# Optimization experiments

Measured on AMD Instinct MI355X. Metric: run time of the kernel, lower is better.

## Reference

```python
import jax, jax.numpy as jnp
import numpy as np

B, S, D, H = 4, 2048, 1024, 16
HD = D // H
FF = 4 * D
EPS = 1e-5


def setup_inputs() -> dict:
    key = jax.random.key(0)
    ks = jax.random.split(key, 12)
    s = lambda fan_in: 1.0 / np.sqrt(fan_in)
    inp = {
        "x": jax.random.normal(ks[0], (B, S, D), dtype=jnp.float32),
        # attention weights stored as (d_in, d_out)
        "Wq": jax.random.normal(ks[1], (D, D), dtype=jnp.float32) * s(D),
        "Wk": jax.random.normal(ks[2], (D, D), dtype=jnp.float32) * s(D),
        "Wv": jax.random.normal(ks[3], (D, D), dtype=jnp.float32) * s(D),
        "Wo": jax.random.normal(ks[4], (D, D), dtype=jnp.float32) * s(D),
        "bo": jnp.zeros((D,), dtype=jnp.float32),
        # feed-forward
        "W1": jax.random.normal(ks[5], (D, FF), dtype=jnp.float32) * s(D),
        "b1": jnp.zeros((FF,), dtype=jnp.float32),
        "W2": jax.random.normal(ks[6], (FF, D), dtype=jnp.float32) * s(FF),
        "b2": jnp.zeros((D,), dtype=jnp.float32),
        # layernorms
        "g1": jnp.ones((D,), dtype=jnp.float32),
        "be1": jnp.zeros((D,), dtype=jnp.float32),
        "g2": jnp.ones((D,), dtype=jnp.float32),
        "be2": jnp.zeros((D,), dtype=jnp.float32),
    }
    return inp


def _layernorm(x, gamma, beta):
    mean = jnp.mean(x, axis=-1, keepdims=True)
    var = jnp.mean(jnp.square(x - mean), axis=-1, keepdims=True)  # unbiased=False
    return gamma * (x - mean) / jnp.sqrt(var + EPS) + beta


def _gelu_tanh(x):
    c = jnp.sqrt(jnp.asarray(2.0 / jnp.pi, dtype=x.dtype))
    return 0.5 * x * (1.0 + jnp.tanh(c * (x + 0.044715 * x * x * x)))


def _block(x, Wq, Wk, Wv, Wo, bo, W1, b1, W2, b2, g1, be1, g2, be2):
    # --- pre-LN causal multi-head attention ---
    shortcut = x
    h = _layernorm(x, g1, be1)
    q = (h @ Wq).reshape(B, S, H, HD).transpose(0, 2, 1, 3)  # [B,H,S,HD]
    k = (h @ Wk).reshape(B, S, H, HD).transpose(0, 2, 1, 3)
    v = (h @ Wv).reshape(B, S, H, HD).transpose(0, 2, 1, 3)
    scores = jnp.einsum("bhqd,bhkd->bhqk", q, k)
    causal = jnp.tril(jnp.ones((S, S), dtype=bool))  # True = keep
    scores = jnp.where(causal, scores, -jnp.inf)
    attn = jax.nn.softmax(scores / jnp.sqrt(jnp.asarray(HD, scores.dtype)), axis=-1)
    ctx = jnp.einsum("bhqk,bhkd->bqhd", attn, v).reshape(B, S, D)
    x = ctx @ Wo + bo + shortcut
    # --- pre-LN GELU MLP ---
    shortcut = x
    h = _layernorm(x, g2, be2)
    h = _gelu_tanh(h @ W1 + b1) @ W2 + b2
    return h + shortcut


def reference(x, Wq, Wk, Wv, Wo, bo, W1, b1, W2, b2, g1, be1, g2, be2):
    return _block(x, Wq, Wk, Wv, Wo, bo, W1, b1, W2, b2, g1, be1, g2, be2)
```

## Files before the change

### kernel.cpp

```cpp
#include <hip/hip_runtime.h>
#include <cstdint>

#define B_   4
#define S_   2048
#define D_   1024
#define H_   16
#define HD_  64
#define FF_  4096
#define MTOK 8192

typedef short s16x8 __attribute__((ext_vector_type(8), may_alias));
typedef float f32x4 __attribute__((ext_vector_type(4)));
typedef unsigned short u16x4 __attribute__((ext_vector_type(4), may_alias));
typedef unsigned short u16x8 __attribute__((ext_vector_type(8), may_alias));

#define GLD_LDS16(g, l)                                                  \
  __builtin_amdgcn_global_load_lds(                                      \
      (__attribute__((address_space(1))) void*)(g),                      \
      (__attribute__((address_space(3))) void*)(l), 16, 0, 0)

__device__ __forceinline__ unsigned short f2bf(float f) {
  unsigned u = __float_as_uint(f);
  unsigned r = 0x7fffu + ((u >> 16) & 1u);
  return (unsigned short)((u + r) >> 16);
}

__global__ __launch_bounds__(256) void k_transpose(const float* __restrict__ in,
                                                   unsigned short* __restrict__ out,
                                                   int R, int C) {
  __shared__ float tile[32][33];
  int tx = threadIdx.x, ty = threadIdx.y;
  int c0 = blockIdx.x * 32, r0 = blockIdx.y * 32;
#pragma unroll
  for (int j = 0; j < 4; ++j)
    tile[ty + j * 8][tx] = in[(size_t)(r0 + ty + j * 8) * C + (c0 + tx)];
  __syncthreads();
#pragma unroll
  for (int j = 0; j < 4; ++j)
    out[(size_t)(c0 + ty + j * 8) * R + (r0 + tx)] = f2bf(tile[tx][ty + j * 8]);
}

__global__ __launch_bounds__(256) void k_layernorm(const float* __restrict__ x,
                                                   const float* __restrict__ g,
                                                   const float* __restrict__ be,
                                                   unsigned short* __restrict__ out) {
  int row = blockIdx.x, t = threadIdx.x;
  const float4* xr = (const float4*)(x + (size_t)row * D_);
  float4 v = xr[t];
  float s = v.x + v.y + v.z + v.w;
  float q = v.x * v.x + v.y * v.y + v.z * v.z + v.w * v.w;
#pragma unroll
  for (int o = 1; o < 64; o <<= 1) { s += __shfl_xor(s, o); q += __shfl_xor(q, o); }
  __shared__ float red[8];
  int wid = t >> 6;
  if ((t & 63) == 0) { red[wid * 2] = s; red[wid * 2 + 1] = q; }
  __syncthreads();
  s = red[0] + red[2] + red[4] + red[6];
  q = red[1] + red[3] + red[5] + red[7];
  float mean = s * (1.0f / D_);
  float rstd = rsqrtf(q * (1.0f / D_) - mean * mean + 1e-5f);
  float4 gv = ((const float4*)g)[t];
  float4 bv = ((const float4*)be)[t];
  u16x4 o4;
  o4[0] = f2bf(gv.x * (v.x - mean) * rstd + bv.x);
  o4[1] = f2bf(gv.y * (v.y - mean) * rstd + bv.y);
  o4[2] = f2bf(gv.z * (v.z - mean) * rstd + bv.z);
  o4[3] = f2bf(gv.w * (v.w - mean) * rstd + bv.w);
  *(u16x4*)(out + (size_t)row * D_ + t * 4) = o4;
}

template <int MODE>
__global__ __launch_bounds__(512, 2) void k_gemm8p(
    const unsigned short* __restrict__ A, const unsigned short* __restrict__ Bt,
    const float* __restrict__ bias,
    unsigned short* __restrict__ outb,
    int M, int N, int K) {
  __shared__ __align__(16) unsigned short smem[8 * 8192];
  unsigned short* const Rs = smem;

  const int tid = threadIdx.x;
  const int wid = tid >> 6, lane = tid & 63;
  const int l16 = lane & 15, lg = lane >> 4;
  const int wr = wid >> 2, wc = wid & 3;
  const int nwg = gridDim.x * gridDim.y;
  const int id = blockIdx.y * gridDim.x + blockIdx.x;
  const int swz = (id & 7) * (nwg >> 3) + (id >> 3);
  const int m0 = (swz / gridDim.x) * 256, n0 = (swz % gridDim.x) * 256;

  f32x4 acc[8][4];
#pragma unroll
  for (int m = 0; m < 8; ++m)
#pragma unroll
    for (int n = 0; n < 4; ++n) acc[m][n] = (f32x4)0.0f;

  const int sRow = tid >> 3;
  const int sC = (((tid & 7) ^ (sRow & 7)) << 3);
  const unsigned short* aS0 = A + (size_t)(m0 + sRow) * K + sC;
  const unsigned short* aS1 = A + (size_t)(m0 + 64 + sRow) * K + sC;
  const unsigned short* aS2 = A + (size_t)(m0 + 128 + sRow) * K + sC;
  const unsigned short* aS3 = A + (size_t)(m0 + 192 + sRow) * K + sC;
  const unsigned short* bS0 = Bt + (size_t)(n0 + sRow) * K + sC;
  const unsigned short* bS1 = Bt + (size_t)(n0 + 64 + sRow) * K + sC;
  const unsigned short* bS2 = Bt + (size_t)(n0 + 128 + sRow) * K + sC;
  const unsigned short* bS3 = Bt + (size_t)(n0 + 192 + sRow) * K + sC;
  const int d0 = tid * 16, d1 = tid * 16 + 8192;

  const int cS0 = ((lg ^ (l16 & 7)) << 3);
  const int cS1 = (((4 + lg) ^ (l16 & 7)) << 3);

  const int nt = K / 64;

  GLD_LDS16(aS0, (char*)(smem + 0 * 8192) + d0);
  GLD_LDS16(aS1, (char*)(smem + 0 * 8192) + d1);
  GLD_LDS16(bS0, (char*)(smem + 1 * 8192) + d0);
  GLD_LDS16(bS1, (char*)(smem + 1 * 8192) + d1);
  GLD_LDS16(bS2, (char*)(smem + 2 * 8192) + d0);
  GLD_LDS16(bS3, (char*)(smem + 2 * 8192) + d1);
  GLD_LDS16(aS2, (char*)(smem + 3 * 8192) + d0);
  GLD_LDS16(aS3, (char*)(smem + 3 * 8192) + d1);
  asm volatile("s_waitcnt vmcnt(4)" ::: "memory");
  __builtin_amdgcn_sched_barrier(0);
  __builtin_amdgcn_s_barrier();

#define PHASE(P, WSTR, DOSTAGE)                                                \
  {                                                                            \
    constexpr int mq_ = (P) >> 1, nh_ = (P) & 1;                               \
    const unsigned short* Au = smem + ((kt & 1) * 4 + (mq_ ? 3 : 0)) * 8192;   \
    const unsigned short* Bu = smem + ((kt & 1) * 4 + 1 + nh_) * 8192;         \
    s16x8 af[4][2], bf[2][2];                                                  \
    _Pragma("unroll")                                                          \
    for (int m4 = 0; m4 < 4; ++m4) {                                           \
      const unsigned short* pr_ = Au + (wr * 64 + m4 * 16 + l16) * 64;         \
      af[m4][0] = *(const s16x8*)(pr_ + cS0);                                  \
      af[m4][1] = *(const s16x8*)(pr_ + cS1);                                  \
    }                                                                          \
    _Pragma("unroll")                                                          \
    for (int n2 = 0; n2 < 2; ++n2) {                                           \
      const unsigned short* pr_ = Bu + (wc * 32 + n2 * 16 + l16) * 64;         \
      bf[n2][0] = *(const s16x8*)(pr_ + cS0);                                  \
      bf[n2][1] = *(const s16x8*)(pr_ + cS1);                                  \
    }                                                                          \
    if (DOSTAGE) {                                                             \
      char* dst_ = (char*)(smem + (((kt + 1) & 1) * 4 + (P)) * 8192);          \
      const size_t ko_ = (size_t)(kt + 1) * 64;                                \
      if constexpr ((P) == 0) {                                                \
        GLD_LDS16(aS0 + ko_, dst_ + d0); GLD_LDS16(aS1 + ko_, dst_ + d1);      \
      } else if constexpr ((P) == 1) {                                         \
        GLD_LDS16(bS0 + ko_, dst_ + d0); GLD_LDS16(bS1 + ko_, dst_ + d1);      \
      } else if constexpr ((P) == 2) {                                         \
        GLD_LDS16(bS2 + ko_, dst_ + d0); GLD_LDS16(bS3 + ko_, dst_ + d1);      \
      } else {                                                                 \
        GLD_LDS16(aS2 + ko_, dst_ + d0); GLD_LDS16(aS3 + ko_, dst_ + d1);      \
      }                                                                        \
    }                                                                          \
    asm volatile("s_waitcnt lgkmcnt(0)" ::: "memory");                         \
    __builtin_amdgcn_sched_barrier(0);                                         \
    __builtin_amdgcn_s_setprio(1);                                             \
    _Pragma("unroll")                                                          \
    for (int m4 = 0; m4 < 4; ++m4)                                             \
      _Pragma("unroll")                                                        \
      for (int n2 = 0; n2 < 2; ++n2) {                                         \
        acc[mq_ * 4 + m4][nh_ * 2 + n2] = __builtin_amdgcn_mfma_f32_16x16x32_bf16( \
            af[m4][0], bf[n2][0], acc[mq_ * 4 + m4][nh_ * 2 + n2], 0, 0, 0);   \
        acc[mq_ * 4 + m4][nh_ * 2 + n2] = __builtin_amdgcn_mfma_f32_16x16x32_bf16( \
            af[m4][1], bf[n2][1], acc[mq_ * 4 + m4][nh_ * 2 + n2], 0, 0, 0);   \
      }                                                                        \
    __builtin_amdgcn_s_setprio(0);                                             \
    asm volatile("s_waitcnt vmcnt(" WSTR ")" ::: "memory");                    \
    __builtin_amdgcn_sched_barrier(0);                                         \
    __builtin_amdgcn_s_barrier();                                              \
  }

  for (int kt = 0; kt < nt - 1; ++kt) {
    PHASE(0, "4", true)
    PHASE(1, "4", true)
    PHASE(2, "4", true)
    PHASE(3, "4", true)
  }
  {
    const int kt = nt - 1;
    PHASE(0, "2", false)
    PHASE(1, "0", false)
    PHASE(2, "0", false)
    PHASE(3, "0", false)
  }
#undef PHASE

#define RM_FLUSH8(DSTPTR, NSTRIDE, COLBASE, XFORM)                             \
  {                                                                            \
    _Pragma("unroll")                                                          \
    for (int pr = 0; pr < 4; ++pr) {                                           \
      if (wr == (pr & 1)) {                                                    \
        const int mb_ = (pr >> 1) * 4;                                         \
        _Pragma("unroll")                                                      \
        for (int nn = 0; nn < 4; ++nn) {                                       \
          const int col = (nn >> 1) * 128 + wc * 32 + (nn & 1) * 16 + l16;     \
          _Pragma("unroll")                                                    \
          for (int m4 = 0; m4 < 4; ++m4) {                                     \
            _Pragma("unroll")                                                  \
            for (int r = 0; r < 4; ++r) {                                      \
              float xv = acc[mb_ + m4][nn][r];                                 \
              XFORM;                                                           \
              Rs[(m4 * 16 + lg * 4 + r) * 264 + col] = f2bf(xv);               \
            }                                                                  \
          }                                                                    \
        }                                                                      \
      }                                                                        \
      __syncthreads();                                                         \
      const int row_l = tid >> 3;                                              \
      _Pragma("unroll")                                                        \
      for (int j = 0; j < 4; ++j) {                                            \
        const int c = (tid & 7) * 4 + j;                                       \
        u16x8 vv = *(const u16x8*)(Rs + row_l * 264 + c * 8);                  \
        *(u16x8*)((DSTPTR) + (size_t)(m0 + pr * 64 + row_l) * (NSTRIDE) +      \
                  (COLBASE) + c * 8) = vv;                                     \
      }                                                                        \
      if (pr < 3) __syncthreads();                                             \
    }                                                                          \
  }

  if constexpr (MODE == 1) {
    RM_FLUSH8(outb, N, n0, {
      xv += bias[n0 + col];
      float uu = 0.7978845608028654f * (xv + 0.044715f * xv * xv * xv);
      xv = xv * __builtin_amdgcn_rcpf(1.0f + __builtin_amdgcn_exp2f(uu * -2.885390081777927f));
    });
    return;
  }

  if constexpr (MODE == 3) {
    unsigned short* qout = outb;
    unsigned short* kout = outb + (size_t)MTOK * D_;
    unsigned short* vout = outb + 2 * (size_t)MTOK * D_;
    if (n0 < 1024) {
      RM_FLUSH8(qout, D_, n0, { xv *= 0.125f; });
    } else if (n0 < 2048) {
      RM_FLUSH8(kout, D_, n0 - 1024, {});
    } else {
      const int vbase = (m0 >> 11) * 1024 + (n0 - 2048);
      const int srow0 = m0 & 2047;
#pragma unroll
      for (int cg = 0; cg < 4; ++cg) {
        if ((wc >> 1) == (cg & 1)) {
          const int nhh = (cg >> 1) * 2;
#pragma unroll
          for (int n2 = 0; n2 < 2; ++n2) {
            const int colL = (wc & 1) * 32 + n2 * 16 + l16;
#pragma unroll
            for (int m = 0; m < 8; ++m) {
              const int rowL = (m >> 2) * 128 + wr * 64 + (m & 3) * 16 + lg * 4;
              u16x4 pk;
#pragma unroll
              for (int r = 0; r < 4; ++r) pk[r] = f2bf(acc[m][nhh + n2][r]);
              *(u16x4*)(Rs + colL * 264 + rowL) = pk;
            }
          }
        }
        __syncthreads();
        const int colf = tid >> 3;
#pragma unroll
        for (int j = 0; j < 4; ++j) {
          u16x8 vv = *(const u16x8*)(Rs + colf * 264 + (tid & 7) * 32 + j * 8);
          *(u16x8*)(vout + (size_t)(vbase + cg * 64 + colf) * S_ + srow0 +
                    (tid & 7) * 32 + j * 8) = vv;
        }
        if (cg < 3) __syncthreads();
      }
    }
    return;
  }
#undef RM_FLUSH8
}

template <int MODE>
__global__ __launch_bounds__(512, 2) void k_gemmdp(
    const unsigned short* __restrict__ A, const unsigned short* __restrict__ Bt,
    const float* __restrict__ bias, const float* __restrict__ resid,
    unsigned short* __restrict__ outb, float* __restrict__ outf,
    int M, int N, int K) {
  constexpr int BM = 128, BN = 256, BK = 64;
  constexpr int AE = BM * BK;
  constexpr int BE = BN * BK;
  constexpr int BUF_E = AE + BE;
  __shared__ __align__(16) unsigned short smem[3 * BUF_E];

  const int tid = threadIdx.x;
  const int wid = tid >> 6, lane = tid & 63;
  const int l16 = lane & 15, lg = lane >> 4;
  const int wr = wid >> 2, wc = wid & 3;
  const int nwg = gridDim.x * gridDim.y;
  const int id = blockIdx.y * gridDim.x + blockIdx.x;
  const int swz = (id & 7) * (nwg >> 3) + (id >> 3);
  const int m0 = (swz / gridDim.x) * BM, n0 = (swz % gridDim.x) * BN;

  f32x4 acc[4][4];
#pragma unroll
  for (int m = 0; m < 4; ++m)
#pragma unroll
    for (int n = 0; n < 4; ++n) acc[m][n] = (f32x4)0.0f;

  const unsigned short* aSrc[2]; int aDstB[2];
  const unsigned short* bSrc[4]; int bDstB[4];
#pragma unroll
  for (int g = 0; g < 2; ++g) {
    int q = g * 512 + tid, row = q >> 3, c = q & 7;
    aSrc[g] = A + (size_t)(m0 + row) * K + ((c ^ (row & 7)) << 3);
    aDstB[g] = q * 16;
  }
#pragma unroll
  for (int g = 0; g < 4; ++g) {
    int q = g * 512 + tid, row = q >> 3, c = q & 7;
    bSrc[g] = Bt + (size_t)(n0 + row) * K + ((c ^ (row & 7)) << 3);
    bDstB[g] = q * 16;
  }
  int cSw[2];
  cSw[0] = ((lg) ^ (l16 & 7)) * 8;
  cSw[1] = ((4 + lg) ^ (l16 & 7)) * 8;
  const int aRow = (wr * 64 + l16) * BK;
  const int bRow = (wc * 64 + l16) * BK;

#define STAGE(ti)                                                              \
  {                                                                            \
    const int _b = (ti) % 3;                                                   \
    char* _pa = (char*)(smem + _b * BUF_E);                                    \
    char* _pb = (char*)(smem + _b * BUF_E + AE);                               \
    const int _kt = (ti) * BK;                                                 \
    _Pragma("unroll")                                                          \
    for (int g = 0; g < 2; ++g) GLD_LDS16(aSrc[g] + _kt, _pa + aDstB[g]);      \
    _Pragma("unroll")                                                          \
    for (int g = 0; g < 4; ++g) GLD_LDS16(bSrc[g] + _kt, _pb + bDstB[g]);      \
  }

  const int nt = K / BK;
  STAGE(0); STAGE(1);
  asm volatile("s_waitcnt vmcnt(6)" ::: "memory");
  __builtin_amdgcn_sched_barrier(0);
  __builtin_amdgcn_s_barrier();

  for (int i = 0; i < nt; ++i) {
    if (i + 2 < nt) STAGE(i + 2);
    const unsigned short* pa = smem + (i % 3) * BUF_E + aRow;
    const unsigned short* pb = smem + (i % 3) * BUF_E + AE + bRow;
    s16x8 af[4][2], bfr[4][2];
#pragma unroll
    for (int m = 0; m < 4; ++m) {
      af[m][0] = *(const s16x8*)(pa + m * 16 * BK + cSw[0]);
      af[m][1] = *(const s16x8*)(pa + m * 16 * BK + cSw[1]);
    }
#pragma unroll
    for (int n = 0; n < 4; ++n) {
      bfr[n][0] = *(const s16x8*)(pb + n * 16 * BK + cSw[0]);
      bfr[n][1] = *(const s16x8*)(pb + n * 16 * BK + cSw[1]);
    }
    asm volatile("s_waitcnt lgkmcnt(0)" ::: "memory");
    __builtin_amdgcn_sched_barrier(0);
    __builtin_amdgcn_s_setprio(1);
#pragma unroll
    for (int m = 0; m < 4; ++m)
#pragma unroll
      for (int n = 0; n < 4; ++n) {
        acc[m][n] = __builtin_amdgcn_mfma_f32_16x16x32_bf16(af[m][0], bfr[n][0], acc[m][n], 0, 0, 0);
        acc[m][n] = __builtin_amdgcn_mfma_f32_16x16x32_bf16(af[m][1], bfr[n][1], acc[m][n], 0, 0, 0);
      }
    __builtin_amdgcn_s_setprio(0);
    if (i < nt - 2) {
      asm volatile("s_waitcnt vmcnt(6)" ::: "memory");
    } else if (i == nt - 2) {
      asm volatile("s_waitcnt vmcnt(0)" ::: "memory");
    }
    __builtin_amdgcn_sched_barrier(0);
    __builtin_amdgcn_s_barrier();
  }
#undef STAGE

  if constexpr (MODE == 2) {
#pragma unroll
    for (int n = 0; n < 4; ++n) {
      const int col = n0 + wc * 64 + n * 16 + l16;
      const float bv = bias[col];
#pragma unroll
      for (int m = 0; m < 4; ++m)
#pragma unroll
        for (int r = 0; r < 4; ++r) {
          const int row = m0 + wr * 64 + m * 16 + lg * 4 + r;
          outf[(size_t)row * N + col] = acc[m][n][r] + bv + resid[(size_t)row * N + col];
        }
    }
  }
  (void)outb;
}

__global__ __launch_bounds__(256, 3) void k_attn(
    const unsigned short* __restrict__ qg, const unsigned short* __restrict__ kg,
    const unsigned short* __restrict__ vtg, unsigned short* __restrict__ ctx) {
  const int id = blockIdx.x;
  const int bh = (id & 7) + 8 * (id >> 7);
  const int p  = (id >> 3) & 15;
  const int qtA = p, qtB = 31 - p;
  const int tid = threadIdx.x, wid = tid >> 6, lane = tid & 63;
  const int l16 = lane & 15, lg = lane >> 4;
  __shared__ __align__(16) unsigned short Ks[2][64 * 64];
  __shared__ __align__(16) unsigned short Vs[2][64 * 64];
  __shared__ __align__(16) unsigned short Ps[4][2][16 * 72];

  const size_t headoff = (size_t)(bh >> 4) * ((size_t)S_ * D_) + (size_t)(bh & 15) * HD_;
  const unsigned short* Kb = kg + headoff;
  const unsigned short* Vt = vtg + (size_t)bh * ((size_t)HD_ * S_);

  const int qrowA = qtA * 64 + wid * 16 + l16;
  const int qrowB = qtB * 64 + wid * 16 + l16;
  s16x8 qfA0 = *(const s16x8*)(qg + headoff + (size_t)qrowA * D_ + lg * 8);
  s16x8 qfA1 = *(const s16x8*)(qg + headoff + (size_t)qrowA * D_ + 32 + lg * 8);
  s16x8 qfB0 = *(const s16x8*)(qg + headoff + (size_t)qrowB * D_ + lg * 8);
  s16x8 qfB1 = *(const s16x8*)(qg + headoff + (size_t)qrowB * D_ + 32 + lg * 8);

  f32x4 oA[4], oB[4];
#pragma unroll
  for (int n = 0; n < 4; ++n) { oA[n] = (f32x4)0.0f; oB[n] = (f32x4)0.0f; }
  float lsumA[4] = {0.f, 0.f, 0.f, 0.f};
  float lsumB[4] = {0.f, 0.f, 0.f, 0.f};
  unsigned short* psA = &Ps[wid][0][0];
  unsigned short* psB = &Ps[wid][1][0];
  const int myrowA = qtA * 64 + wid * 16 + lg * 4;
  const int myrowB = qtB * 64 + wid * 16 + lg * 4;
  const float L2E = 1.4426950408889634f;

  const unsigned short* kSrc[2];
  const unsigned short* vSrc[2];
  int dstOff[2];
#pragma unroll
  for (int i = 0; i < 2; ++i) {
    int chunk = (i * 4 + wid) * 64 + lane;
    int row = chunk >> 3, pc = chunk & 7;
    int scol = (pc ^ (row & 7)) * 8;
    kSrc[i] = Kb + (size_t)row * D_ + scol;
    vSrc[i] = Vt + (size_t)row * S_ + scol;
    dstOff[i] = (i * 4 + wid) * 1024;
  }

#pragma unroll
  for (int i = 0; i < 2; ++i) {
    GLD_LDS16(kSrc[i], (char*)Ks[0] + dstOff[i]);
    GLD_LDS16(vSrc[i], (char*)Vs[0] + dstOff[i]);
  }
  __syncthreads();

  for (int t = 0; t <= qtB; ++t) {
    const int cur = t & 1;
    const int kv0 = t * 64;
    const bool doA = (t <= qtA);
    if (t < qtB) {
      const int kvn = kv0 + 64;
#pragma unroll
      for (int i = 0; i < 2; ++i) {
        GLD_LDS16(kSrc[i] + (size_t)kvn * D_, (char*)Ks[cur ^ 1] + dstOff[i]);
        GLD_LDS16(vSrc[i] + kvn, (char*)Vs[cur ^ 1] + dstOff[i]);
      }
    }
    const unsigned short* Kc = Ks[cur];
    const unsigned short* Vc = Vs[cur];
    s16x8 kf0[4], kf1[4];
#pragma unroll
    for (int n = 0; n < 4; ++n) {
      int srow = n * 16 + l16, sw = srow & 7;
      kf0[n] = *(const s16x8*)(Kc + srow * 64 + (lg ^ sw) * 8);
      kf1[n] = *(const s16x8*)(Kc + srow * 64 + ((4 + lg) ^ sw) * 8);
    }
    f32x4 saA[4], saB[4];
    if (doA) {
#pragma unroll
      for (int n = 0; n < 4; ++n) {
        saA[n] = (f32x4)0.0f;
        saA[n] = __builtin_amdgcn_mfma_f32_16x16x32_bf16(qfA0, kf0[n], saA[n], 0, 0, 0);
        saA[n] = __builtin_amdgcn_mfma_f32_16x16x32_bf16(qfA1, kf1[n], saA[n], 0, 0, 0);
      }
    }
#pragma unroll
    for (int n = 0; n < 4; ++n) {
      saB[n] = (f32x4)0.0f;
      saB[n] = __builtin_amdgcn_mfma_f32_16x16x32_bf16(qfB0, kf0[n], saB[n], 0, 0, 0);
      saB[n] = __builtin_amdgcn_mfma_f32_16x16x32_bf16(qfB1, kf1[n], saB[n], 0, 0, 0);
    }
    if (doA) {
      const bool mask = (t == qtA);
#pragma unroll
      for (int r = 0; r < 4; ++r)
#pragma unroll
        for (int n = 0; n < 4; ++n) {
          float pv = exp2f((saA[n][r] - 12.0f) * L2E);
          if (mask && (kv0 + n * 16 + l16) > (myrowA + r)) pv = 0.0f;
          lsumA[r] += pv;
          psA[(lg * 4 + r) * 72 + n * 16 + l16] = f2bf(pv);
        }
    }
    {
      const bool mask = (t == qtB);
#pragma unroll
      for (int r = 0; r < 4; ++r)
#pragma unroll
        for (int n = 0; n < 4; ++n) {
          float pv = exp2f((saB[n][r] - 12.0f) * L2E);
          if (mask && (kv0 + n * 16 + l16) > (myrowB + r)) pv = 0.0f;
          lsumB[r] += pv;
          psB[(lg * 4 + r) * 72 + n * 16 + l16] = f2bf(pv);
        }
    }
    s16x8 vf0[4], vf1[4];
#pragma unroll
    for (int n = 0; n < 4; ++n) {
      int srow = n * 16 + l16, sw = srow & 7;
      vf0[n] = *(const s16x8*)(Vc + srow * 64 + (lg ^ sw) * 8);
      vf1[n] = *(const s16x8*)(Vc + srow * 64 + ((4 + lg) ^ sw) * 8);
    }
    __builtin_amdgcn_sched_barrier(0);
    asm volatile("s_waitcnt lgkmcnt(0)" ::: "memory");
    __builtin_amdgcn_sched_barrier(0);
    {
      s16x8 paB0 = *(const s16x8*)(psB + l16 * 72 + lg * 8);
      s16x8 paB1 = *(const s16x8*)(psB + l16 * 72 + 32 + lg * 8);
#pragma unroll
      for (int n = 0; n < 4; ++n) {
        oB[n] = __builtin_amdgcn_mfma_f32_16x16x32_bf16(paB0, vf0[n], oB[n], 0, 0, 0);
        oB[n] = __builtin_amdgcn_mfma_f32_16x16x32_bf16(paB1, vf1[n], oB[n], 0, 0, 0);
      }
      if (doA) {
        s16x8 paA0 = *(const s16x8*)(psA + l16 * 72 + lg * 8);
        s16x8 paA1 = *(const s16x8*)(psA + l16 * 72 + 32 + lg * 8);
#pragma unroll
        for (int n = 0; n < 4; ++n) {
          oA[n] = __builtin_amdgcn_mfma_f32_16x16x32_bf16(paA0, vf0[n], oA[n], 0, 0, 0);
          oA[n] = __builtin_amdgcn_mfma_f32_16x16x32_bf16(paA1, vf1[n], oA[n], 0, 0, 0);
        }
      }
    }
    __syncthreads();
  }

#pragma unroll
  for (int r = 0; r < 4; ++r) {
    float la = lsumA[r], lb = lsumB[r];
    la += __shfl_xor(la, 1); lb += __shfl_xor(lb, 1);
    la += __shfl_xor(la, 2); lb += __shfl_xor(lb, 2);
    la += __shfl_xor(la, 4); lb += __shfl_xor(lb, 4);
    la += __shfl_xor(la, 8); lb += __shfl_xor(lb, 8);
    float ia = 1.0f / la, ib = 1.0f / lb;
#pragma unroll
    for (int n = 0; n < 4; ++n) {
      ctx[headoff + (size_t)(myrowA + r) * D_ + n * 16 + l16] = f2bf(oA[n][r] * ia);
      ctx[headoff + (size_t)(myrowB + r) * D_ + n * 16 + l16] = f2bf(oB[n][r] * ib);
    }
  }
}

extern "C" void kernel_launch(void* const* d_in, const int* in_sizes, int n_in,
                              void* d_out, int out_size, void* d_ws, size_t ws_size,
                              hipStream_t stream) {
  (void)in_sizes; (void)n_in; (void)out_size; (void)ws_size;
  const float* x   = (const float*)d_in[0];
  const float* Wq  = (const float*)d_in[1];
  const float* Wk  = (const float*)d_in[2];
  const float* Wv  = (const float*)d_in[3];
  const float* Wo  = (const float*)d_in[4];
  const float* bo  = (const float*)d_in[5];
  const float* W1  = (const float*)d_in[6];
  const float* b1  = (const float*)d_in[7];
  const float* W2  = (const float*)d_in[8];
  const float* b2  = (const float*)d_in[9];
  const float* g1  = (const float*)d_in[10];
  const float* be1 = (const float*)d_in[11];
  const float* g2  = (const float*)d_in[12];
  const float* be2 = (const float*)d_in[13];
  float* out = (float*)d_out;

  char* w = (char*)d_ws;
  const size_t MB = 1ull << 20;
  unsigned short* wqkvT = (unsigned short*)(w + 0 * MB);
  unsigned short* woT   = (unsigned short*)(w + 6 * MB);
  unsigned short* w1T   = (unsigned short*)(w + 8 * MB);
  unsigned short* w2T   = (unsigned short*)(w + 16 * MB);
  unsigned short* hb    = (unsigned short*)(w + 24 * MB);
  float*          x2    = (float*)(w + 40 * MB);
  unsigned short* qkv   = (unsigned short*)(w + 72 * MB);
  unsigned short* qb    = qkv;
  unsigned short* kb    = qkv + (size_t)MTOK * D_;
  unsigned short* vbT   = qkv + 2 * (size_t)MTOK * D_;
  unsigned short* cxb   = (unsigned short*)(w + 120 * MB);
  unsigned short* act   = (unsigned short*)(w + 72 * MB);

  dim3 tb(32, 8);
  k_transpose<<<dim3(32, 32), tb, 0, stream>>>(Wq, wqkvT, 1024, 1024);
  k_transpose<<<dim3(32, 32), tb, 0, stream>>>(Wk, wqkvT + 1024 * 1024, 1024, 1024);
  k_transpose<<<dim3(32, 32), tb, 0, stream>>>(Wv, wqkvT + 2048 * 1024, 1024, 1024);
  k_transpose<<<dim3(32, 32), tb, 0, stream>>>(Wo, woT, 1024, 1024);
  k_transpose<<<dim3(128, 32), tb, 0, stream>>>(W1, w1T, 1024, 4096);
  k_transpose<<<dim3(32, 128), tb, 0, stream>>>(W2, w2T, 4096, 1024);

  k_layernorm<<<MTOK, 256, 0, stream>>>(x, g1, be1, hb);

  k_gemm8p<3><<<dim3(12, 32), 512, 0, stream>>>(hb, wqkvT, nullptr, qkv, MTOK, 3072, 1024);

  k_attn<<<1024, 256, 0, stream>>>(qb, kb, vbT, cxb);

  k_gemmdp<2><<<dim3(4, 64), 512, 0, stream>>>(cxb, woT, bo, x, nullptr, x2, MTOK, 1024, 1024);

  k_layernorm<<<MTOK, 256, 0, stream>>>(x2, g2, be2, hb);

  k_gemm8p<1><<<dim3(16, 32), 512, 0, stream>>>(hb, w1T, b1, act, MTOK, 4096, 1024);
  k_gemmdp<2><<<dim3(4, 64), 512, 0, stream>>>(act, w2T, b2, x2, nullptr, out, MTOK, 1024, 4096);
}
```

Before: 423.1 us.

## Restructure GEMM main loop to reuse register fragments and deepen LDS prefetch

Rewrites the 256x256 GEMM k-loop as a two-k-tile unrolled schedule over eight LDS slots. A and B fragments are kept in registers and reused across quadrant MFMAs, so the old per-phase reload of both operands is gone. Global-to-LDS staging now runs up to seven slots ahead, with vmcnt(6) waits. The aim is fewer LDS reads and more load/compute overlap, at the cost of extra register pressure and a more fragile slot and wait-count schedule.

```diff
diff --git a/kernel.cpp b/kernel.cpp
--- a/kernel.cpp
+++ b/kernel.cpp
@@ -108,83 +108,114 @@
   const int cS0 = ((lg ^ (l16 & 7)) << 3);
   const int cS1 = (((4 + lg) ^ (l16 & 7)) << 3);
 
-  const int nt = K / 64;
-
-  GLD_LDS16(aS0, (char*)(smem + 0 * 8192) + d0);
-  GLD_LDS16(aS1, (char*)(smem + 0 * 8192) + d1);
-  GLD_LDS16(bS0, (char*)(smem + 1 * 8192) + d0);
-  GLD_LDS16(bS1, (char*)(smem + 1 * 8192) + d1);
-  GLD_LDS16(bS2, (char*)(smem + 2 * 8192) + d0);
-  GLD_LDS16(bS3, (char*)(smem + 2 * 8192) + d1);
-  GLD_LDS16(aS2, (char*)(smem + 3 * 8192) + d0);
-  GLD_LDS16(aS3, (char*)(smem + 3 * 8192) + d1);
-  asm volatile("s_waitcnt vmcnt(4)" ::: "memory");
-  __builtin_amdgcn_sched_barrier(0);
-  __builtin_amdgcn_s_barrier();
-
-#define PHASE(P, WSTR, DOSTAGE)                                                \
+#define READ_A(SLOT)                                                           \
+  _Pragma("unroll")                                                            \
+  for (int m4 = 0; m4 < 4; ++m4) {                                             \
+    const unsigned short* pr_ = smem + (SLOT) * 8192 + (wr * 64 + m4 * 16 + l16) * 64; \
+    af[m4][0] = *(const s16x8*)(pr_ + cS0);                                    \
+    af[m4][1] = *(const s16x8*)(pr_ + cS1);                                    \
+  }
+#define READ_B(SLOT, DEST)                                                     \
+  _Pragma("unroll")                                                            \
+  for (int n2 = 0; n2 < 2; ++n2) {                                             \
+    const unsigned short* pr_ = smem + (SLOT) * 8192 + (wc * 32 + n2 * 16 + l16) * 64; \
+    DEST[n2][0] = *(const s16x8*)(pr_ + cS0);                                  \
+    DEST[n2][1] = *(const s16x8*)(pr_ + cS1);                                  \
+  }
+#define STAGE2(SLOT, P0_, P1_, KOFF)                                           \
   {                                                                            \
-    constexpr int mq_ = (P) >> 1, nh_ = (P) & 1;                               \
-    const unsigned short* Au = smem + ((kt & 1) * 4 + (mq_ ? 3 : 0)) * 8192;   \
-    const unsigned short* Bu = smem + ((kt & 1) * 4 + 1 + nh_) * 8192;         \
-    s16x8 af[4][2], bf[2][2];                                                  \
-    _Pragma("unroll")                                                          \
-    for (int m4 = 0; m4 < 4; ++m4) {                                           \
-      const unsigned short* pr_ = Au + (wr * 64 + m4 * 16 + l16) * 64;         \
-      af[m4][0] = *(const s16x8*)(pr_ + cS0);                                  \
-      af[m4][1] = *(const s16x8*)(pr_ + cS1);                                  \
-    }                                                                          \
+    char* dst_ = (char*)(smem + (SLOT) * 8192);                                \
+    GLD_LDS16((P0_) + (KOFF), dst_ + d0);                                      \
+    GLD_LDS16((P1_) + (KOFF), dst_ + d1);                                      \
+  }
+#define MFMAQ(MQ, NH, AF, BF)                                                  \
+  __builtin_amdgcn_s_setprio(1);                                               \
+  _Pragma("unroll")                                                            \
+  for (int m4 = 0; m4 < 4; ++m4)                                               \
     _Pragma("unroll")                                                          \
     for (int n2 = 0; n2 < 2; ++n2) {                                           \
-      const unsigned short* pr_ = Bu + (wc * 32 + n2 * 16 + l16) * 64;         \
-      bf[n2][0] = *(const s16x8*)(pr_ + cS0);                                  \
-      bf[n2][1] = *(const s16x8*)(pr_ + cS1);                                  \
+      acc[(MQ) * 4 + m4][(NH) * 2 + n2] = __builtin_amdgcn_mfma_f32_16x16x32_bf16( \
+          AF[m4][0], BF[n2][0], acc[(MQ) * 4 + m4][(NH) * 2 + n2], 0, 0, 0);   \
+      acc[(MQ) * 4 + m4][(NH) * 2 + n2] = __builtin_amdgcn_mfma_f32_16x16x32_bf16( \
+          AF[m4][1], BF[n2][1], acc[(MQ) * 4 + m4][(NH) * 2 + n2], 0, 0, 0);   \
     }                                                                          \
-    if (DOSTAGE) {                                                             \
-      char* dst_ = (char*)(smem + (((kt + 1) & 1) * 4 + (P)) * 8192);          \
-      const size_t ko_ = (size_t)(kt + 1) * 64;                                \
-      if constexpr ((P) == 0) {                                                \
-        GLD_LDS16(aS0 + ko_, dst_ + d0); GLD_LDS16(aS1 + ko_, dst_ + d1);      \
-      } else if constexpr ((P) == 1) {                                         \
-        GLD_LDS16(bS0 + ko_, dst_ + d0); GLD_LDS16(bS1 + ko_, dst_ + d1);      \
-      } else if constexpr ((P) == 2) {                                         \
-        GLD_LDS16(bS2 + ko_, dst_ + d0); GLD_LDS16(bS3 + ko_, dst_ + d1);      \
-      } else {                                                                 \
-        GLD_LDS16(aS2 + ko_, dst_ + d0); GLD_LDS16(aS3 + ko_, dst_ + d1);      \
-      }                                                                        \
-    }                                                                          \
-    asm volatile("s_waitcnt lgkmcnt(0)" ::: "memory");                         \
-    __builtin_amdgcn_sched_barrier(0);                                         \
-    __builtin_amdgcn_s_setprio(1);                                             \
-    _Pragma("unroll")                                                          \
-    for (int m4 = 0; m4 < 4; ++m4)                                             \
-      _Pragma("unroll")                                                        \
-      for (int n2 = 0; n2 < 2; ++n2) {                                         \
-        acc[mq_ * 4 + m4][nh_ * 2 + n2] = __builtin_amdgcn_mfma_f32_16x16x32_bf16( \
-            af[m4][0], bf[n2][0], acc[mq_ * 4 + m4][nh_ * 2 + n2], 0, 0, 0);   \
-        acc[mq_ * 4 + m4][nh_ * 2 + n2] = __builtin_amdgcn_mfma_f32_16x16x32_bf16( \
-            af[m4][1], bf[n2][1], acc[mq_ * 4 + m4][nh_ * 2 + n2], 0, 0, 0);   \
-      }                                                                        \
-    __builtin_amdgcn_s_setprio(0);                                             \
-    asm volatile("s_waitcnt vmcnt(" WSTR ")" ::: "memory");                    \
-    __builtin_amdgcn_sched_barrier(0);                                         \
-    __builtin_amdgcn_s_barrier();                                              \
-  }
-
-  for (int kt = 0; kt < nt - 1; ++kt) {
-    PHASE(0, "4", true)
-    PHASE(1, "4", true)
-    PHASE(2, "4", true)
-    PHASE(3, "4", true)
-  }
-  {
-    const int kt = nt - 1;
-    PHASE(0, "2", false)
-    PHASE(1, "0", false)
-    PHASE(2, "0", false)
-    PHASE(3, "0", false)
-  }
-#undef PHASE
+  __builtin_amdgcn_s_setprio(0);
+#define LGK0                                                                   \
+  asm volatile("s_waitcnt lgkmcnt(0)" ::: "memory");                           \
+  __builtin_amdgcn_sched_barrier(0);
+#define BAR_ONLY                                                               \
+  __builtin_amdgcn_sched_barrier(0);                                           \
+  __builtin_amdgcn_s_barrier();
+
+  STAGE2(0, aS0, aS1, 0)
+  STAGE2(1, bS0, bS1, 0)
+  STAGE2(2, bS2, bS3, 0)
+  STAGE2(3, aS2, aS3, 0)
+  STAGE2(4, aS0, aS1, 64)
+  STAGE2(5, bS0, bS1, 64)
+  STAGE2(6, bS2, bS3, 64)
+  asm volatile("s_waitcnt vmcnt(0)" ::: "memory");
+  BAR_ONLY
+
+  const int nt2 = K / 128;
+  for (int j = 0; j < nt2; ++j) {
+    const bool stg = (j < nt2 - 1);
+    const size_t k1 = (size_t)(2 * j + 1) * 64;
+    const size_t k2 = (size_t)(2 * j + 2) * 64;
+    const size_t k3 = (size_t)(2 * j + 3) * 64;
+    s16x8 af[4][2], blo[2][2], bhi[2][2];
+    READ_A(0)
+    READ_B(1, blo)
+    STAGE2(7, aS2, aS3, k1)
+    LGK0
+    MFMAQ(0, 0, af, blo)
+    BAR_ONLY
+    READ_B(2, bhi)
+    if (stg) STAGE2(0, aS0, aS1, k2)
+    LGK0
+    MFMAQ(0, 1, af, bhi)
+    BAR_ONLY
+    READ_A(3)
+    if (stg) STAGE2(1, bS0, bS1, k2)
+    LGK0
+    MFMAQ(1, 0, af, blo)
+    BAR_ONLY
+    if (stg) STAGE2(2, bS2, bS3, k2)
+    MFMAQ(1, 1, af, bhi)
+    if (stg) { asm volatile("s_waitcnt vmcnt(6)" ::: "memory"); }
+    else     { asm volatile("s_waitcnt vmcnt(0)" ::: "memory"); }
+    BAR_ONLY
+    READ_A(4)
+    READ_B(5, blo)
+    if (stg) STAGE2(3, aS2, aS3, k2)
+    LGK0
+    MFMAQ(0, 0, af, blo)
+    BAR_ONLY
+    READ_B(6, bhi)
+    if (stg) STAGE2(4, aS0, aS1, k3)
+    LGK0
+    MFMAQ(0, 1, af, bhi)
+    BAR_ONLY
+    READ_A(7)
+    if (stg) STAGE2(5, bS0, bS1, k3)
+    LGK0
+    MFMAQ(1, 0, af, blo)
+    BAR_ONLY
+    if (stg) {
+      STAGE2(6, bS2, bS3, k3)
+      MFMAQ(1, 1, af, bhi)
+      asm volatile("s_waitcnt vmcnt(6)" ::: "memory");
+    } else {
+      MFMAQ(1, 1, af, bhi)
+    }
+    BAR_ONLY
+  }
+#undef READ_A
+#undef READ_B
+#undef STAGE2
+#undef MFMAQ
+#undef LGK0
+#undef BAR_ONLY
 
 #define RM_FLUSH8(DSTPTR, NSTRIDE, COLBASE, XFORM)                             \
   {                                                                            \
```

Result: faster. 411.3 us (median of 2 runs) (-2.8%).
